# Kernel tuning notes

Measured on AMD Instinct MI355X. Metric: run time of the kernel, lower is better.

The kernel has to match this reference:

```python
import jax, jax.numpy as jnp
import numpy as np

N = 16        # state dim n
M = 8         # control dim m
T = 50        # time_steps
DT = 0.01     # delta_t
SQRT_DT = DT ** 0.5
GAMMA = 0.1
SIGMA = 0.2
TAU = 0.5
H = 10        # hidden width of subnets
BATCH = 32768


def _mlp(params, x):
    W1, b1, W2, b2, W3, b3 = params
    h = jnp.tanh(x @ W1 + b1)
    h = jnp.tanh(h @ W2 + b2)
    return h @ W3 + b3


def setup_inputs() -> dict:
    key = jax.random.key(0)
    ks = jax.random.split(key, 32)

    def dense(k, i, o):
        return (jax.random.normal(k, (i, o), jnp.float32) / np.float32(np.sqrt(i)))

    inp = {
        'dw': jax.random.normal(ks[0], (T, BATCH, 1), jnp.float32) * SQRT_DT,
        'X0': jax.random.uniform(ks[1], (BATCH, N), jnp.float32),
        'A': dense(ks[2], N, N),
        'Bmat': dense(ks[3], N, M),
        'Cmat': dense(ks[4], N, N),
        'Dmat': dense(ks[5], N, M),
        # phi: (n+1) -> 10 -> 10 -> m
        'phi_W1': dense(ks[6], N + 1, H), 'phi_b1': jnp.zeros((H,), jnp.float32),
        'phi_W2': dense(ks[7], H, H),     'phi_b2': jnp.zeros((H,), jnp.float32),
        'phi_W3': dense(ks[8], H, M),     'phi_b3': jnp.zeros((M,), jnp.float32),
        # Z: (n+1) -> 10 -> 10 -> n
        'Z_W1': dense(ks[9], N + 1, H),   'Z_b1': jnp.zeros((H,), jnp.float32),
        'Z_W2': dense(ks[10], H, H),      'Z_b2': jnp.zeros((H,), jnp.float32),
        'Z_W3': dense(ks[11], H, N),      'Z_b3': jnp.zeros((N,), jnp.float32),
        # Y0: n -> 10 -> 10 -> n
        'Y0_W1': dense(ks[12], N, H),     'Y0_b1': jnp.zeros((H,), jnp.float32),
        'Y0_W2': dense(ks[13], H, H),     'Y0_b2': jnp.zeros((H,), jnp.float32),
        'Y0_W3': dense(ks[14], H, N),     'Y0_b3': jnp.zeros((N,), jnp.float32),
    }
    return inp


def reference(dw, X0, A, Bmat, Cmat, Dmat,
              phi_W1, phi_b1, phi_W2, phi_b2, phi_W3, phi_b3,
              Z_W1, Z_b1, Z_W2, Z_b2, Z_W3, Z_b3,
              Y0_W1, Y0_b1, Y0_W2, Y0_b2, Y0_W3, Y0_b3):
    phi_p = (phi_W1, phi_b1, phi_W2, phi_b2, phi_W3, phi_b3)
    Z_p = (Z_W1, Z_b1, Z_W2, Z_b2, Z_W3, Z_b3)
    Y0_p = (Y0_W1, Y0_b1, Y0_W2, Y0_b2, Y0_W3, Y0_b3)

    B = X0.shape[0]
    Y = _mlp(Y0_p, X0)                              # [B, n]
    t_grid = jnp.arange(T, dtype=X0.dtype) * DT     # [T]
    w_trap = jnp.ones((T,), X0.dtype).at[1:-1].set(2.0)  # trapezoid weights

    def step(carry, xs):
        X, Yc, lc = carry
        dwi, t, w = xs                              # dwi: [B,1]
        state = jnp.concatenate(
            [jnp.broadcast_to(t, (B, 1)).astype(X.dtype), X], axis=1)  # [B, n+1]
        Zv = _mlp(Z_p, state)                       # [B, n]
        u = _mlp(phi_p, state)                      # [B, m] (project = identity)
        # b_mult(M, x) == x @ M.T
        drift_X = X @ A.T + u @ Bmat.T + GAMMA      # [B, n]
        diffusion_X = X @ Cmat.T + u @ Dmat.T + SIGMA
        drift_Y = -(Yc @ A + Zv @ Cmat + X)         # f_x(X,u) = X
        # stop_recording branch: gradient of dH / pre_phi
        dH = Yc @ Bmat + Zv @ Dmat + u              # f_u(X,u) = u -> [B, m]
        pre_phi = jax.lax.stop_gradient(u - TAU * dH)
        Xn = X + drift_X * DT + dwi * diffusion_X
        Yn = Yc + drift_Y * DT + dwi * Zv
        lc = lc + 0.5 * DT * w * jnp.sum(jnp.square(u - pre_phi), axis=1)
        return (Xn, Yn, lc), None

    init = (X0, Y, jnp.zeros((B,), X0.dtype))
    (X, Y, loss_control), _ = jax.lax.scan(step, init, (dw, t_grid, w_trap))
    loss_bsde = jnp.sum(jnp.square(Y - X), axis=1)  # g_x(X) = X
    return jnp.stack([jnp.mean(loss_bsde), jnp.mean(loss_control)])
```

## Files before the change

kernel.cpp:

```cpp
#include <hip/hip_runtime.h>

namespace {

typedef float v4f __attribute__((ext_vector_type(4)));
typedef _Float16 half4 __attribute__((ext_vector_type(4)));
typedef __fp16 fp16x2 __attribute__((ext_vector_type(2)));
typedef unsigned int uint32;

constexpr int   kB     = 32768;
constexpr int   kT     = 50;
constexpr float kDT    = 0.01f;
constexpr float kGamma = 0.1f;
constexpr float kSigma = 0.2f;
constexpr float kTau   = 0.5f;
constexpr float kA     = 2.8853900817779268f;

constexpr int kNFrag      = 17;
constexpr int kFragDwords = kNFrag * 128;
constexpr int kBiasFloats = 15 * 16;

__device__ __forceinline__ float fexp2(float x) {
#if __has_builtin(__builtin_amdgcn_exp2f)
  return __builtin_amdgcn_exp2f(x);
#else
  return exp2f(x);
#endif
}

__device__ __forceinline__ float fact(float x) {
  return __builtin_amdgcn_rcpf(fexp2(x) + 1.0f);
}

__device__ __forceinline__ v4f act4(v4f a) {
  v4f r;
  r[0] = fact(a[0]); r[1] = fact(a[1]);
  r[2] = fact(a[2]); r[3] = fact(a[3]);
  return r;
}

__device__ __forceinline__ uint32 pk2rtn(float a, float b) {
  union { _Float16 h[2]; uint32 u; } z;
  z.h[0] = (_Float16)a; z.h[1] = (_Float16)b;
  return z.u;
}

__global__ __launch_bounds__(64) void prep_kernel(
    const float* __restrict__ A,   const float* __restrict__ Bm,
    const float* __restrict__ Cm,  const float* __restrict__ Dm,
    const float* __restrict__ pW1, const float* __restrict__ pb1,
    const float* __restrict__ pW2, const float* __restrict__ pb2,
    const float* __restrict__ pW3, const float* __restrict__ pb3,
    const float* __restrict__ zW1, const float* __restrict__ zb1,
    const float* __restrict__ zW2, const float* __restrict__ zb2,
    const float* __restrict__ zW3, const float* __restrict__ zb3,
    const float* __restrict__ yW1, const float* __restrict__ yb1,
    const float* __restrict__ yW2, const float* __restrict__ yb2,
    const float* __restrict__ yW3, const float* __restrict__ yb3,
    uint32* __restrict__ ws)
{
  const int tid = threadIdx.x;
  const int blk = blockIdx.x;

  auto sum10 = [](const float* W, int stride, int mm) {
    float s = 0.f;
#pragma unroll
    for (int j = 0; j < 10; ++j) s += W[j * stride + mm];
    return s;
  };

  if (blk < kNFrag) {
    const int m = tid & 15, q = tid >> 4;
    const int p = blk;

    auto wv = [&](int k) -> float {
      float s = 0.f;
      switch (p) {
        case 0:  return (m < 10) ? kA * yW1[k * 10 + m] : 0.f;
        case 1:  return (m < 10 && k < 10) ? -2.f * kA * yW2[k * 10 + m] : 0.f;
        case 2:  return (k < 10) ? -2.f * yW3[k * 16 + m] : 0.f;
        case 3:  return (m < 10) ? kA * zW1[(k + 1) * 10 + m] : 0.f;
        case 4:  return (m < 10) ? kA * pW1[(k + 1) * 10 + m] : 0.f;
        case 5:  return (m < 10 && k < 10) ? -2.f * kA * zW2[k * 10 + m] : 0.f;
        case 6:  return (m < 10 && k < 10) ? -2.f * kA * pW2[k * 10 + m] : 0.f;
        case 7:  return (k < 10) ? -2.f * zW3[k * 16 + m] : 0.f;
        case 8:  return (m < 8 && k < 10) ? -2.f * pW3[k * 8 + m] : 0.f;
        case 9:  return A[m * 16 + k];
        case 11: return Cm[m * 16 + k];
        case 13: return A[k * 16 + m];
        case 15: return (m < 8) ? Bm[k * 8 + m] : 0.f;
        case 10:
          if (k >= 10) return 0.f;
#pragma unroll
          for (int qq = 0; qq < 8; ++qq) s += Bm[m * 8 + qq] * pW3[k * 8 + qq];
          return -2.f * s;
        case 12:
          if (k >= 10) return 0.f;
#pragma unroll
          for (int qq = 0; qq < 8; ++qq) s += Dm[m * 8 + qq] * pW3[k * 8 + qq];
          return -2.f * s;
        case 14:
          if (k >= 10) return 0.f;
#pragma unroll
          for (int kk = 0; kk < 16; ++kk) s += zW3[k * 16 + kk] * Cm[kk * 16 + m];
          return -2.f * s;
        case 16:
          if (m >= 8 || k >= 10) return 0.f;
#pragma unroll
          for (int kk = 0; kk < 16; ++kk) s += zW3[k * 16 + kk] * Dm[kk * 8 + m];
          return -2.f * s;
      }
      return 0.f;
    };

    const int k0 = 4 * q;
    ws[p * 128 + tid * 2]     = pk2rtn(wv(k0),     wv(k0 + 1));
    ws[p * 128 + tid * 2 + 1] = pk2rtn(wv(k0 + 2), wv(k0 + 3));
  } else {
    float* bsf = (float*)(ws + kFragDwords);
    auto b3p = [&](int q) { return pb3[q] + sum10(pW3, 8, q); };
    auto b3z = [&](int k) { return zb3[k] + sum10(zW3, 16, k); };
    auto bval = [&](int a, int mm) -> float {
      const bool m10 = mm < 10;
      float s = 0.f;
      switch (a) {
        case 0:  return m10 ? kA * yb1[mm] : 0.f;
        case 1:  return m10 ? kA * (yb2[mm] + sum10(yW2, 10, mm)) : 0.f;
        case 2:  return yb3[mm] + sum10(yW3, 16, mm);
        case 3:  return m10 ? kA * (zb2[mm] + sum10(zW2, 10, mm)) : 0.f;
        case 4:  return m10 ? kA * (pb2[mm] + sum10(pW2, 10, mm)) : 0.f;
        case 5:  return b3z(mm);
        case 6:  return (mm < 8) ? b3p(mm) : 0.f;
        case 7:  return m10 ? kA * zW1[mm] : 0.f;
        case 8:  return m10 ? kA * zb1[mm] : 0.f;
        case 9:  return m10 ? kA * pW1[mm] : 0.f;
        case 10: return m10 ? kA * pb1[mm] : 0.f;
        case 11:
#pragma unroll
          for (int q = 0; q < 8; ++q) s += Bm[mm * 8 + q] * b3p(q);
          return s;
        case 12:
#pragma unroll
          for (int q = 0; q < 8; ++q) s += Dm[mm * 8 + q] * b3p(q);
          return s;
        case 13:
#pragma unroll
          for (int k = 0; k < 16; ++k) s += Cm[k * 16 + mm] * b3z(k);
          return s;
        case 14:
          if (mm >= 8) return 0.f;
#pragma unroll
          for (int k = 0; k < 16; ++k) s += Dm[k * 8 + mm] * b3z(k);
          return s;
      }
      return 0.f;
    };
    for (int j = tid; j < kBiasFloats; j += 64) {
      bsf[j] = bval(j >> 4, j & 15);
    }
  }
}

__global__ __launch_bounds__(128)
__attribute__((amdgpu_waves_per_eu(2, 4)))
void bsde_kernel(const float* __restrict__ dw, const float* __restrict__ X0,
                 const uint32* __restrict__ wsu, float* __restrict__ out)
{
  const int tid  = threadIdx.x;
  const int w    = tid >> 6;
  const int lane = tid & 63;
  const int col  = lane & 15;
  const int quad = lane >> 4;
  const int e    = blockIdx.x * 16 + col;
  const int bq   = quad * 4;

  __shared__ float sx[2][64][4];
  __shared__ float su[2][64][4];

  auto ldfrag = [&](int p) -> half4 {
    union { uint2 u; half4 h; } z;
    z.u = *(const uint2*)(wsu + p * 128 + lane * 2);
    return z.h;
  };
  const float* bsf = (const float*)(wsu + kFragDwords);

  const half4 aL1 = ldfrag(w ? 4 : 3);
  const half4 aL2 = ldfrag(w ? 6 : 5);
  const half4 aL3 = ldfrag(w ? 8 : 7);
  const half4 aE1 = ldfrag(w ? 9 : 13);
  const half4 aE2 = ldfrag(w ? 11 : 15);
  const half4 aW1 = ldfrag(w ? 10 : 14);
  const half4 aW2 = ldfrag(w ? 12 : 16);
  const v4f c2 = *(const v4f*)&bsf[(w ? 4 : 3) * 16 + bq];
  const v4f c3 = *(const v4f*)&bsf[(w ? 6 : 5) * 16 + bq];
  const v4f vt = *(const v4f*)&bsf[(w ? 9 : 7) * 16 + bq];
  const v4f vb = *(const v4f*)&bsf[(w ? 10 : 8) * 16 + bq];
  v4f s1c, s2c;
  {
    const v4f ba = *(const v4f*)&bsf[(w ? 11 : 13) * 16 + bq];
    const v4f bb = *(const v4f*)&bsf[(w ? 12 : 14) * 16 + bq];
#pragma unroll
    for (int r = 0; r < 4; ++r) {
      s1c[r] = w ? (kGamma + ba[r]) : ba[r];
      s2c[r] = w ? (kSigma + bb[r]) : bb[r];
    }
  }

  auto pk4 = [](v4f a) -> half4 {
    union { fp16x2 p[2]; half4 h; } z;
    z.p[0] = __builtin_amdgcn_cvt_pkrtz(a[0], a[1]);
    z.p[1] = __builtin_amdgcn_cvt_pkrtz(a[2], a[3]);
    return z.h;
  };
  auto mm4 = [](half4 a, half4 b, v4f c) -> v4f {
    return __builtin_amdgcn_mfma_f32_16x16x16f16(a, b, c, 0, 0, 0);
  };

  v4f x4 = *(const v4f*)&X0[e * 16 + bq];
  half4 xB = pk4(x4);
  v4f y4 = {0.f, 0.f, 0.f, 0.f};
  half4 yB = pk4(y4);
  if (w == 0) {
    const half4 a0 = ldfrag(0), a1 = ldfrag(1), a2 = ldfrag(2);
    const v4f cy1 = *(const v4f*)&bsf[0 * 16 + bq];
    const v4f cy2 = *(const v4f*)&bsf[1 * 16 + bq];
    const v4f cy3 = *(const v4f*)&bsf[2 * 16 + bq];
    v4f h = mm4(a0, xB, cy1);
    v4f g = mm4(a1, pk4(act4(h)), cy2);
    y4    = mm4(a2, pk4(act4(g)), cy3);
    yB    = pk4(y4);
  }

  float dwc = dw[e];
  float lcp = 0.0f;

#pragma unroll 1
  for (int i = 0; i <= kT; ++i) {
    const int idx = w ? (i + 1) : i;
    const float dwn = (idx < kT) ? dw[idx * kB + e] : 0.0f;

    if (w) {
      if (i < kT) {
        const float tv = (float)i * kDT;
        v4f c1;
#pragma unroll
        for (int r = 0; r < 4; ++r) c1[r] = vb[r] + tv * vt[r];
        v4f h = mm4(aL1, xB, c1);
        half4 hB = pk4(act4(h));
        v4f g = mm4(aL2, hB, c2);
        half4 gB = pk4(act4(g));
        v4f u = mm4(aL3, gB, c3);
        *(v4f*)&su[i & 1][lane][0] = u;
        v4f s1 = mm4(aE1, xB, s1c);
        v4f s2 = mm4(aE2, xB, s2c);
        v4f dx = mm4(aW1, gB, s1);
        v4f fx = mm4(aW2, gB, s2);
        v4f Xn;
#pragma unroll
        for (int r = 0; r < 4; ++r) Xn[r] = x4[r] + kDT * dx[r] + dwc * fx[r];
        *(v4f*)&sx[i & 1][lane][0] = Xn;
        x4 = Xn;
        xB = pk4(x4);
      }
    } else {
      if (i >= 1) {
        const int s = i - 1;
        const float tv = (float)s * kDT;
        const float wt = (s == 0 || s == kT - 1) ? 1.0f : 2.0f;
        v4f c1;
#pragma unroll
        for (int r = 0; r < 4; ++r) c1[r] = vb[r] + tv * vt[r];
        v4f h = mm4(aL1, xB, c1);
        half4 hB = pk4(act4(h));
        v4f g = mm4(aL2, hB, c2);
        half4 gB = pk4(act4(g));
        v4f zv = mm4(aL3, gB, c3);
        v4f s1yc;
#pragma unroll
        for (int r = 0; r < 4; ++r) s1yc[r] = x4[r] + s1c[r];
        v4f s1y = mm4(aE1, yB, s1yc);
        v4f s2y = mm4(aE2, yB, s2c);
        v4f dy = mm4(aW1, gB, s1y);
        v4f dh = mm4(aW2, gB, s2y);
        const v4f uu = *(const v4f*)&su[s & 1][lane][0];
        v4f Yn;
        float ss = 0.0f;
#pragma unroll
        for (int r = 0; r < 4; ++r) {
          Yn[r] = y4[r] - kDT * dy[r] + dwc * zv[r];
          float d = dh[r] + uu[r];
          ss += d * d;
        }
        lcp += (0.5f * kDT * kTau * kTau) * wt * ss;
        y4 = Yn;
        yB = pk4(y4);
        x4 = *(const v4f*)&sx[s & 1][lane][0];
        xB = pk4(x4);
      }
    }
    __syncthreads();
    dwc = dwn;
  }

  if (w == 0) {
    float bp = 0.0f;
#pragma unroll
    for (int r = 0; r < 4; ++r) { float d = y4[r] - x4[r]; bp += d * d; }
#pragma unroll
    for (int s = 32; s > 0; s >>= 1) {
      bp  += __shfl_down(bp,  s, 64);
      lcp += __shfl_down(lcp, s, 64);
    }
    if (lane == 0) {
      atomicAdd(&out[0], bp  * (1.0f / (float)kB));
      atomicAdd(&out[1], lcp * (1.0f / (float)kB));
    }
  }
}

}

extern "C" void kernel_launch(void* const* d_in, const int* in_sizes, int n_in,
                              void* d_out, int out_size, void* d_ws, size_t ws_size,
                              hipStream_t stream) {
  (void)in_sizes; (void)n_in; (void)ws_size; (void)out_size;

  const float* dw  = (const float*)d_in[0];
  const float* X0  = (const float*)d_in[1];
  const float* A   = (const float*)d_in[2];
  const float* Bm  = (const float*)d_in[3];
  const float* Cm  = (const float*)d_in[4];
  const float* Dm  = (const float*)d_in[5];
  const float* pW1 = (const float*)d_in[6];
  const float* pb1 = (const float*)d_in[7];
  const float* pW2 = (const float*)d_in[8];
  const float* pb2 = (const float*)d_in[9];
  const float* pW3 = (const float*)d_in[10];
  const float* pb3 = (const float*)d_in[11];
  const float* zW1 = (const float*)d_in[12];
  const float* zb1 = (const float*)d_in[13];
  const float* zW2 = (const float*)d_in[14];
  const float* zb2 = (const float*)d_in[15];
  const float* zW3 = (const float*)d_in[16];
  const float* zb3 = (const float*)d_in[17];
  const float* yW1 = (const float*)d_in[18];
  const float* yb1 = (const float*)d_in[19];
  const float* yW2 = (const float*)d_in[20];
  const float* yb2 = (const float*)d_in[21];
  const float* yW3 = (const float*)d_in[22];
  const float* yb3 = (const float*)d_in[23];
  float* out = (float*)d_out;
  unsigned int* ws = (unsigned int*)d_ws;

  (void)hipMemsetAsync(out, 0, 2 * sizeof(float), stream);

  prep_kernel<<<kNFrag + 1, 64, 0, stream>>>(
      A, Bm, Cm, Dm,
      pW1, pb1, pW2, pb2, pW3, pb3,
      zW1, zb1, zW2, zb2, zW3, zb3,
      yW1, yb1, yW2, yb2, yW3, yb3, ws);

  bsde_kernel<<<kB / 16, 128, 0, stream>>>(dw, X0, ws, out);
}
```

Measured before the change: 185.9 us.

## Merge producer/consumer waves into one wave computing X and Y paths per step

Replaces the two-wave producer/consumer pipeline (one wave advancing X and phi, the other Z and Y, exchanging state via shared memory with a block barrier each step) with a single wave per block that computes both MLPs and both state updates each timestep. This removes the per-step __syncthreads and LDS traffic and exposes two independent MFMA chains for interleaving. In exchange each wave carries twice the weight fragments and serial work, register pressure rises, and the total number of waves is halved.

```diff
diff --git a/kernel.cpp b/kernel.cpp
--- a/kernel.cpp
+++ b/kernel.cpp
@@ -160,21 +160,16 @@
   }
 }
 
-__global__ __launch_bounds__(128)
-__attribute__((amdgpu_waves_per_eu(2, 4)))
+__global__ __launch_bounds__(64)
+__attribute__((amdgpu_waves_per_eu(2, 2)))
 void bsde_kernel(const float* __restrict__ dw, const float* __restrict__ X0,
                  const uint32* __restrict__ wsu, float* __restrict__ out)
 {
-  const int tid  = threadIdx.x;
-  const int w    = tid >> 6;
-  const int lane = tid & 63;
+  const int lane = threadIdx.x;
   const int col  = lane & 15;
   const int quad = lane >> 4;
   const int e    = blockIdx.x * 16 + col;
   const int bq   = quad * 4;
-
-  __shared__ float sx[2][64][4];
-  __shared__ float su[2][64][4];
 
   auto ldfrag = [&](int p) -> half4 {
     union { uint2 u; half4 h; } z;
@@ -183,25 +178,32 @@
   };
   const float* bsf = (const float*)(wsu + kFragDwords);
 
-  const half4 aL1 = ldfrag(w ? 4 : 3);
-  const half4 aL2 = ldfrag(w ? 6 : 5);
-  const half4 aL3 = ldfrag(w ? 8 : 7);
-  const half4 aE1 = ldfrag(w ? 9 : 13);
-  const half4 aE2 = ldfrag(w ? 11 : 15);
-  const half4 aW1 = ldfrag(w ? 10 : 14);
-  const half4 aW2 = ldfrag(w ? 12 : 16);
-  const v4f c2 = *(const v4f*)&bsf[(w ? 4 : 3) * 16 + bq];
-  const v4f c3 = *(const v4f*)&bsf[(w ? 6 : 5) * 16 + bq];
-  const v4f vt = *(const v4f*)&bsf[(w ? 9 : 7) * 16 + bq];
-  const v4f vb = *(const v4f*)&bsf[(w ? 10 : 8) * 16 + bq];
-  v4f s1c, s2c;
+  const half4 aL1z = ldfrag(3),  aL1p = ldfrag(4);
+  const half4 aL2z = ldfrag(5),  aL2p = ldfrag(6);
+  const half4 aL3z = ldfrag(7),  aL3p = ldfrag(8);
+  const half4 aAr  = ldfrag(9),  aCr  = ldfrag(11);
+  const half4 aAc  = ldfrag(13), aBc  = ldfrag(15);
+  const half4 aBWP = ldfrag(10), aDWP = ldfrag(12);
+  const half4 aCWZ = ldfrag(14), aDWZ = ldfrag(16);
+
+  const v4f c2z = *(const v4f*)&bsf[3 * 16 + bq];
+  const v4f c2p = *(const v4f*)&bsf[4 * 16 + bq];
+  const v4f c3z = *(const v4f*)&bsf[5 * 16 + bq];
+  const v4f c3p = *(const v4f*)&bsf[6 * 16 + bq];
+  const v4f vtz = *(const v4f*)&bsf[7 * 16 + bq];
+  const v4f vbz = *(const v4f*)&bsf[8 * 16 + bq];
+  const v4f vtp = *(const v4f*)&bsf[9 * 16 + bq];
+  const v4f vbp = *(const v4f*)&bsf[10 * 16 + bq];
+  v4f s1cx, s2cx, czb, dzb;
   {
-    const v4f ba = *(const v4f*)&bsf[(w ? 11 : 13) * 16 + bq];
-    const v4f bb = *(const v4f*)&bsf[(w ? 12 : 14) * 16 + bq];
+    const v4f bpb = *(const v4f*)&bsf[11 * 16 + bq];
+    const v4f dpb = *(const v4f*)&bsf[12 * 16 + bq];
+    czb = *(const v4f*)&bsf[13 * 16 + bq];
+    dzb = *(const v4f*)&bsf[14 * 16 + bq];
 #pragma unroll
     for (int r = 0; r < 4; ++r) {
-      s1c[r] = w ? (kGamma + ba[r]) : ba[r];
-      s2c[r] = w ? (kSigma + bb[r]) : bb[r];
+      s1cx[r] = kGamma + bpb[r];
+      s2cx[r] = kSigma + dpb[r];
     }
   }
 
@@ -217,9 +219,8 @@
 
   v4f x4 = *(const v4f*)&X0[e * 16 + bq];
   half4 xB = pk4(x4);
-  v4f y4 = {0.f, 0.f, 0.f, 0.f};
-  half4 yB = pk4(y4);
-  if (w == 0) {
+  v4f y4;
+  {
     const half4 a0 = ldfrag(0), a1 = ldfrag(1), a2 = ldfrag(2);
     const v4f cy1 = *(const v4f*)&bsf[0 * 16 + bq];
     const v4f cy2 = *(const v4f*)&bsf[1 * 16 + bq];
@@ -227,93 +228,76 @@
     v4f h = mm4(a0, xB, cy1);
     v4f g = mm4(a1, pk4(act4(h)), cy2);
     y4    = mm4(a2, pk4(act4(g)), cy3);
-    yB    = pk4(y4);
-  }
-
-  float dwc = dw[e];
+  }
+  half4 yB = pk4(y4);
+
   float lcp = 0.0f;
+  float dwv = dw[e];
 
 #pragma unroll 1
-  for (int i = 0; i <= kT; ++i) {
-    const int idx = w ? (i + 1) : i;
-    const float dwn = (idx < kT) ? dw[idx * kB + e] : 0.0f;
-
-    if (w) {
-      if (i < kT) {
-        const float tv = (float)i * kDT;
-        v4f c1;
-#pragma unroll
-        for (int r = 0; r < 4; ++r) c1[r] = vb[r] + tv * vt[r];
-        v4f h = mm4(aL1, xB, c1);
-        half4 hB = pk4(act4(h));
-        v4f g = mm4(aL2, hB, c2);
-        half4 gB = pk4(act4(g));
-        v4f u = mm4(aL3, gB, c3);
-        *(v4f*)&su[i & 1][lane][0] = u;
-        v4f s1 = mm4(aE1, xB, s1c);
-        v4f s2 = mm4(aE2, xB, s2c);
-        v4f dx = mm4(aW1, gB, s1);
-        v4f fx = mm4(aW2, gB, s2);
-        v4f Xn;
-#pragma unroll
-        for (int r = 0; r < 4; ++r) Xn[r] = x4[r] + kDT * dx[r] + dwc * fx[r];
-        *(v4f*)&sx[i & 1][lane][0] = Xn;
-        x4 = Xn;
-        xB = pk4(x4);
-      }
-    } else {
-      if (i >= 1) {
-        const int s = i - 1;
-        const float tv = (float)s * kDT;
-        const float wt = (s == 0 || s == kT - 1) ? 1.0f : 2.0f;
-        v4f c1;
-#pragma unroll
-        for (int r = 0; r < 4; ++r) c1[r] = vb[r] + tv * vt[r];
-        v4f h = mm4(aL1, xB, c1);
-        half4 hB = pk4(act4(h));
-        v4f g = mm4(aL2, hB, c2);
-        half4 gB = pk4(act4(g));
-        v4f zv = mm4(aL3, gB, c3);
-        v4f s1yc;
-#pragma unroll
-        for (int r = 0; r < 4; ++r) s1yc[r] = x4[r] + s1c[r];
-        v4f s1y = mm4(aE1, yB, s1yc);
-        v4f s2y = mm4(aE2, yB, s2c);
-        v4f dy = mm4(aW1, gB, s1y);
-        v4f dh = mm4(aW2, gB, s2y);
-        const v4f uu = *(const v4f*)&su[s & 1][lane][0];
-        v4f Yn;
-        float ss = 0.0f;
-#pragma unroll
-        for (int r = 0; r < 4; ++r) {
-          Yn[r] = y4[r] - kDT * dy[r] + dwc * zv[r];
-          float d = dh[r] + uu[r];
-          ss += d * d;
-        }
-        lcp += (0.5f * kDT * kTau * kTau) * wt * ss;
-        y4 = Yn;
-        yB = pk4(y4);
-        x4 = *(const v4f*)&sx[s & 1][lane][0];
-        xB = pk4(x4);
-      }
+  for (int t = 0; t < kT; ++t) {
+    const float dwn = (t < kT - 1) ? dw[(t + 1) * kB + e] : 0.0f;
+    const float tv  = (float)t * kDT;
+    const float wt  = (t == 0 || t == kT - 1) ? 1.0f : 2.0f;
+
+    v4f s1x = mm4(aAr, xB, s1cx);
+    v4f s2x = mm4(aCr, xB, s2cx);
+    v4f s1yc;
+#pragma unroll
+    for (int r = 0; r < 4; ++r) s1yc[r] = x4[r] + czb[r];
+    v4f s1y = mm4(aAc, yB, s1yc);
+    v4f s2y = mm4(aBc, yB, dzb);
+
+    v4f c1z, c1p;
+#pragma unroll
+    for (int r = 0; r < 4; ++r) {
+      c1z[r] = vbz[r] + tv * vtz[r];
+      c1p[r] = vbp[r] + tv * vtp[r];
     }
-    __syncthreads();
-    dwc = dwn;
-  }
-
-  if (w == 0) {
-    float bp = 0.0f;
-#pragma unroll
-    for (int r = 0; r < 4; ++r) { float d = y4[r] - x4[r]; bp += d * d; }
-#pragma unroll
-    for (int s = 32; s > 0; s >>= 1) {
-      bp  += __shfl_down(bp,  s, 64);
-      lcp += __shfl_down(lcp, s, 64);
+
+    v4f hz = mm4(aL1z, xB, c1z);
+    v4f hp = mm4(aL1p, xB, c1p);
+    v4f gz = mm4(aL2z, pk4(act4(hz)), c2z);
+    v4f gp = mm4(aL2p, pk4(act4(hp)), c2p);
+    half4 gzB = pk4(act4(gz));
+    half4 gpB = pk4(act4(gp));
+
+    v4f zv = mm4(aL3z, gzB, c3z);
+    v4f uu = mm4(aL3p, gpB, c3p);
+
+    v4f dx = mm4(aBWP, gpB, s1x);
+    v4f fx = mm4(aDWP, gpB, s2x);
+    v4f dy = mm4(aCWZ, gzB, s1y);
+    v4f dh = mm4(aDWZ, gzB, s2y);
+
+    float ss = 0.0f;
+    v4f Xn, Yn;
+#pragma unroll
+    for (int r = 0; r < 4; ++r) {
+      Xn[r] = x4[r] + kDT * dx[r] + dwv * fx[r];
+      Yn[r] = y4[r] - kDT * dy[r] + dwv * zv[r];
+      float d = dh[r] + uu[r];
+      ss += d * d;
     }
-    if (lane == 0) {
-      atomicAdd(&out[0], bp  * (1.0f / (float)kB));
-      atomicAdd(&out[1], lcp * (1.0f / (float)kB));
-    }
+    lcp += (0.5f * kDT * kTau * kTau) * wt * ss;
+    x4 = Xn; y4 = Yn;
+    xB = pk4(x4);
+    yB = pk4(y4);
+    dwv = dwn;
+  }
+
+  float bp = 0.0f;
+#pragma unroll
+  for (int r = 0; r < 4; ++r) { float d = y4[r] - x4[r]; bp += d * d; }
+
+#pragma unroll
+  for (int s = 32; s > 0; s >>= 1) {
+    bp  += __shfl_down(bp,  s, 64);
+    lcp += __shfl_down(lcp, s, 64);
+  }
+  if (lane == 0) {
+    atomicAdd(&out[0], bp  * (1.0f / (float)kB));
+    atomicAdd(&out[1], lcp * (1.0f / (float)kB));
   }
 }
 
@@ -359,5 +343,5 @@
       zW1, zb1, zW2, zb2, zW3, zb3,
       yW1, yb1, yW2, yb2, yW3, yb3, ws);
 
-  bsde_kernel<<<kB / 16, 128, 0, stream>>>(dw, X0, ws, out);
-}
+  bsde_kernel<<<kB / 16, 64, 0, stream>>>(dw, X0, ws, out);
+}
```

Result: slower. 196.5 us (+5.7%).
